# Performance work log

Hardware: AMD Instinct MI355X
Metric: run time of the kernel (lower is better)

The kernel has to match this reference:

```python
import jax, jax.numpy as jnp
import numpy as np

EPS = 1e-8

def _cosine(a, b):
    # a: (b,h,s,d), b: (b,1,1,d) -> (b,h,s). torch eps semantics: clamp each norm.
    num = jnp.sum(a * b, axis=-1)
    na = jnp.maximum(jnp.linalg.norm(a, axis=-1), EPS)
    nb = jnp.maximum(jnp.linalg.norm(b, axis=-1), EPS)
    return num / (na * nb)

def setup_inputs() -> dict:
    B, H, S, DH, DM = 2, 16, 2048, 64, 1024
    key = jax.random.key(0)
    ks = jax.random.split(key, 8)
    queries = jax.random.normal(ks[0], (B, H, S, DH), dtype=jnp.float32)
    keys = jax.random.normal(ks[1], (B, H, S, DH), dtype=jnp.float32)
    context = jax.random.normal(ks[2], (B, DM), dtype=jnp.float32)
    prev_state = jax.random.normal(ks[3], (B, S, DH), dtype=jnp.float32)
    # causal mask (1 = keep, 0 = masked), shape (B,1,S,S)
    attention_mask = jnp.broadcast_to(jnp.tril(jnp.ones((S, S), dtype=jnp.int32)), (B, 1, S, S))
    # learned params (Linear weights stored torch-style as (out, in))
    cfm_ctx_w = jax.random.normal(ks[4], (DH, DM), dtype=jnp.float32) / np.sqrt(DM)
    cfm_state_w = jax.random.normal(ks[5], (DH, DH), dtype=jnp.float32) / np.sqrt(DH)
    afm_ctx_w = jax.random.normal(ks[6], (DH, DM), dtype=jnp.float32) / np.sqrt(DM)
    cfm_scale = jnp.full((1,), 0.1, dtype=jnp.float32)
    afm_scale = jnp.full((1,), 0.1, dtype=jnp.float32)
    alpha = jnp.asarray(0.1, dtype=jnp.float32)
    beta = jnp.asarray(0.1, dtype=jnp.float32)
    return dict(queries=queries, keys=keys, context=context, prev_state=prev_state,
                attention_mask=attention_mask, cfm_ctx_w=cfm_ctx_w, cfm_state_w=cfm_state_w,
                cfm_scale=cfm_scale, afm_ctx_w=afm_ctx_w, afm_scale=afm_scale,
                alpha=alpha, beta=beta)

def reference(queries, keys, context, prev_state, attention_mask,
              cfm_ctx_w, cfm_state_w, cfm_scale, afm_ctx_w, afm_scale, alpha, beta):
    B, H, S, DH = queries.shape
    # QK^T / sqrt(d_k): (b,h,s,s)
    attn_scores = jnp.einsum('bhqd,bhkd->bhqk', queries, keys) / jnp.sqrt(jnp.asarray(DH, queries.dtype))
    # ---- CFM ----
    cfm_ctx = (context @ cfm_ctx_w.T)[:, None, None, :]            # (b,1,1,dh)
    witt = _cosine(keys, cfm_ctx)                                   # (b,h,s)
    state = (prev_state @ cfm_state_w.T)[:, None, :, :]             # (b,1,s,dh)
    hamming = jnp.mean(((keys > 0) != (state > 0)).astype(keys.dtype), axis=-1)  # (b,h,s)
    cfm = ((witt + (1.0 - hamming)) * cfm_scale[0])[:, :, None, :]  # (b,h,1,s)
    # ---- AFM (no key_probs -> uniform entropy 1/S) ----
    afm_ctx = (context @ afm_ctx_w.T)[:, None, None, :]
    contradiction = jax.nn.relu(-_cosine(keys, afm_ctx))            # (b,h,s)
    entropy = jnp.full_like(contradiction, 1.0 / S)
    afm = ((contradiction + entropy) * afm_scale[0])[:, :, None, :]
    composite = attn_scores + alpha * cfm - beta * afm
    composite = jnp.where(attention_mask == 0, -jnp.inf, composite)
    return composite
```

## Files before the change

kernel.cpp:

```cpp
#include <hip/hip_runtime.h>
#include <math.h>

#define BB 2
#define HH 16
#define SS 2048
#define DHD 64
#define DMD 1024
#define EPSF 1e-8f
#define NEG_FILL -1.0e30f

typedef __attribute__((ext_vector_type(8))) short bf16x8;
typedef __attribute__((ext_vector_type(4))) float f32x4;

#define WS_BIAS_F   1024
#define WS_CONV_F   66560
#define CONV_ELEMS  (BB * HH * SS * DHD)
#define GRAN_TOTAL  (CONV_ELEMS / 8)
#define WS_NEEDED_B ((size_t)WS_CONV_F * 4 + (size_t)CONV_ELEMS * 2 * 4)

static __device__ __forceinline__ unsigned short f2bf(float f) {
    unsigned u = __float_as_uint(f);
    u += 0x7FFFu + ((u >> 16) & 1u);
    return (unsigned short)(u >> 16);
}
static __device__ __forceinline__ float bf2f(unsigned short h) {
    return __uint_as_float(((unsigned)h) << 16);
}
static __device__ __forceinline__ void cvt8(const float* p, bf16x8& h8, bf16x8& l8) {
    float4 v0 = *(const float4*)p;
    float4 v1 = *(const float4*)(p + 4);
    float vf[8] = {v0.x, v0.y, v0.z, v0.w, v1.x, v1.y, v1.z, v1.w};
    #pragma unroll
    for (int j = 0; j < 8; ++j) {
        unsigned short h = f2bf(vf[j]);
        h8[j] = (short)h;
        l8[j] = (short)f2bf(vf[j] - bf2f(h));
    }
}

__global__ void ctx_kernel(const float* __restrict__ context,
                           const float* __restrict__ cfm_ctx_w,
                           const float* __restrict__ afm_ctx_w,
                           float* __restrict__ ws) {
    int t = threadIdx.x;
    int b = t >> 7, sel = (t >> 6) & 1, o = t & 63;
    const float* W = sel ? afm_ctx_w : cfm_ctx_w;
    const float4* wrow = (const float4*)(W + o * DMD);
    const float4* crow = (const float4*)(context + b * DMD);
    float acc = 0.f;
    for (int m = 0; m < DMD / 4; ++m) {
        float4 w4 = wrow[m];
        float4 c4 = crow[m];
        acc += w4.x * c4.x + w4.y * c4.y + w4.z * c4.z + w4.w * c4.w;
    }
    ws[b * 128 + sel * 64 + o] = acc;
    float sq = acc * acc;
    for (int off = 32; off >= 1; off >>= 1) sq += __shfl_xor(sq, off);
    if (o == 0) ws[256 + b * 2 + sel] = fmaxf(sqrtf(sq), EPSF);
}

__global__ void bias_kernel(const float* __restrict__ keys,
                            const float* __restrict__ prev_state,
                            const float* __restrict__ cfm_state_w,
                            const float* __restrict__ cfm_scale,
                            const float* __restrict__ afm_scale,
                            const float* __restrict__ alpha_p,
                            const float* __restrict__ beta_p,
                            const float* __restrict__ ws_ctx,
                            float* __restrict__ bias_out) {
    int gid = blockIdx.x * 4 + (threadIdx.x >> 6);
    int b = gid >> 11, s = gid & (SS - 1);
    int l = threadIdx.x & 63;
    const float4* prow = (const float4*)(prev_state + ((size_t)b * SS + s) * DHD);
    const float4* wrow = (const float4*)(cfm_state_w + l * DHD);
    float st = 0.f;
    #pragma unroll
    for (int j = 0; j < DHD / 4; ++j) {
        float4 p4 = prow[j], w4 = wrow[j];
        st += p4.x * w4.x + p4.y * w4.y + p4.z * w4.z + p4.w * w4.w;
    }
    unsigned long long smask = __ballot(st > 0.f);

    int h = l >> 2, q = l & 3, d0 = q * 16;
    int sb = (int)((smask >> d0) & 0xFFFFull);
    const float* krow = keys + (((size_t)(b * HH + h)) * SS + s) * DHD + d0;
    const float* cc = ws_ctx + b * 128 + d0;
    const float* ac = ws_ctx + b * 128 + 64 + d0;
    float v0 = 0.f, v1 = 0.f, v2 = 0.f, mism = 0.f;
    #pragma unroll
    for (int j4 = 0; j4 < 4; ++j4) {
        float4 k4 = *(const float4*)(krow + j4 * 4);
        float4 c4 = *(const float4*)(cc + j4 * 4);
        float4 a4 = *(const float4*)(ac + j4 * 4);
        float kf[4] = {k4.x, k4.y, k4.z, k4.w};
        float cf[4] = {c4.x, c4.y, c4.z, c4.w};
        float af[4] = {a4.x, a4.y, a4.z, a4.w};
        #pragma unroll
        for (int j = 0; j < 4; ++j) {
            float kd = kf[j];
            v0 = fmaf(kd, cf[j], v0);
            v1 = fmaf(kd, af[j], v1);
            v2 = fmaf(kd, kd, v2);
            int bit = (sb >> (j4 * 4 + j)) & 1;
            mism += ((kd > 0.f) != (bit != 0)) ? 1.f : 0.f;
        }
    }
    v0 += __shfl_xor(v0, 1); v0 += __shfl_xor(v0, 2);
    v1 += __shfl_xor(v1, 1); v1 += __shfl_xor(v1, 2);
    v2 += __shfl_xor(v2, 1); v2 += __shfl_xor(v2, 2);
    mism += __shfl_xor(mism, 1); mism += __shfl_xor(mism, 2);
    if (q == 0) {
        float nb_c = ws_ctx[256 + b * 2];
        float nb_a = ws_ctx[256 + b * 2 + 1];
        float al = alpha_p[0] * cfm_scale[0];
        float be = beta_p[0] * afm_scale[0];
        float nk = fmaxf(sqrtf(v2), EPSF);
        float witt = v0 / (nk * nb_c);
        float contra = fmaxf(-(v1 / (nk * nb_a)), 0.f);
        float ham = mism * (1.f / 64.f);
        bias_out[(size_t)(b * HH + h) * SS + s] =
            al * (witt + 1.f - ham) - be * (contra + 1.f / (float)SS);
    }
}

__global__ void conv_kernel(const float* __restrict__ Q,
                            const float* __restrict__ K,
                            unsigned short* __restrict__ wsc) {
    int sel = blockIdx.y;
    const float* src = sel ? K : Q;
    float scale = sel ? 1.f : 0.125f;
    unsigned short* hi = wsc + (size_t)(sel ? 2 : 0) * CONV_ELEMS;
    unsigned short* lo = hi + CONV_ELEMS;
    int gid = blockIdx.x * 256 + threadIdx.x;
    int bh = gid >> 14;
    int rem = gid & 16383;
    int u = rem >> 7, r2 = rem & 127;
    int s = r2 >> 6, r3 = r2 & 63;
    int lg = r3 >> 4, lr = r3 & 15;
    size_t sidx = ((size_t)bh * SS + u * 16 + lr) * DHD + s * 32 + lg * 8;
    float4 a = *(const float4*)(src + sidx);
    float4 b = *(const float4*)(src + sidx + 4);
    float vf[8] = {a.x, a.y, a.z, a.w, b.x, b.y, b.z, b.w};
    bf16x8 h8, l8;
    #pragma unroll
    for (int j = 0; j < 8; ++j) {
        float f = vf[j] * scale;
        unsigned short h = f2bf(f);
        h8[j] = (short)h;
        l8[j] = (short)f2bf(f - bf2f(h));
    }
    *(bf16x8*)(hi + (size_t)gid * 8) = h8;
    *(bf16x8*)(lo + (size_t)gid * 8) = l8;
}

#define MFMA16(A, B, C) __builtin_amdgcn_mfma_f32_16x16x32_bf16(A, B, C, 0, 0, 0)

__global__ __launch_bounds__(256, 2) void band_pc(
    const unsigned short* __restrict__ wsc,
    const float* __restrict__ bias, float* __restrict__ out) {
    int L = blockIdx.x;
    int xcd = L & 7, sL = L >> 3;
    int j = sL & 31;
    int bh = ((sL >> 5) << 3) | xcd;
    int tid = threadIdx.x;
    int w = tid >> 6, l = tid & 63, lr = l & 15, lg = l >> 4;
    int lg4 = lg * 4;

    int chunksA = (j >> 1) + 1;
    int chunksA4 = (chunksA + 3) & ~3;
    int chunksZ = 32 - (j >> 1);
    int chunksZ4 = (chunksZ + 3) & ~3;
    if (chunksZ4 > 32) chunksZ4 = 32;
    int nchunks = chunksZ4;
    int ngroups = nchunks >> 2;
    int mygroupsA = chunksA4 >> 2;
    int fillA = chunksA4 * 64;
    int fillZ = chunksZ4 * 64;
    int rowA = j * 32, rowZ = (63 - j) * 32;
    int fr0 = 4 * (ngroups - mygroupsA);
    if (fr0 > 32) fr0 = 32;

    __shared__ unsigned short KB[2][8192];
    __shared__ float BIASL[2048];
    __shared__ float TR[2][16 * 256];

    const unsigned short* Qh = wsc;
    const unsigned short* Ql = Qh + CONV_ELEMS;
    const unsigned short* Kh = Ql + CONV_ELEMS;
    const unsigned short* Kl = Kh + CONV_ELEMS;
    const float* bias_g = bias + (size_t)bh * SS;
    float* ob = out + (size_t)bh * SS * SS;
    size_t kbase = (size_t)bh * 131072;
    f32x4 fneg = {NEG_FILL, NEG_FILL, NEG_FILL, NEG_FILL};

#define STAGE(cidx, nb) do {                                                 \
    bf16x8 t[8];                                                             \
    _Pragma("unroll")                                                        \
    for (int gi = 0; gi < 8; ++gi) {                                         \
        int g = pw * 8 + gi, u = g >> 2, q = g & 3;                          \
        const unsigned short* src = (q < 2 ? Kh : Kl) + kbase                \
            + (size_t)((cidx) * 4 + u) * 1024 + (q & 1) * 512 + l * 8;       \
        t[gi] = *(const bf16x8*)src;                                         \
    }                                                                        \
    _Pragma("unroll")                                                        \
    for (int gi = 0; gi < 8; ++gi) {                                         \
        int g = pw * 8 + gi, u = g >> 2, q = g & 3;                          \
        *(bf16x8*)&KB[nb][u * 2048 + q * 512 + l * 8] = t[gi];               \
    }                                                                        \
} while (0)

    if (w >= 2) {
        int pw = w - 2;
        #pragma unroll
        for (int i = 0; i < 4; ++i) {
            f32x4 bv = *(const f32x4*)(bias_g + pw * 1024 + i * 256 + l * 4);
            *(f32x4*)&BIASL[pw * 1024 + i * 256 + l * 4] = bv;
        }
        STAGE(0, 0);
        asm volatile("s_waitcnt lgkmcnt(0)" ::: "memory");
        __builtin_amdgcn_sched_barrier(0);
        for (int c = 0; c < nchunks; ++c) {
            __builtin_amdgcn_s_barrier();
            if (c + 1 < nchunks) {
                STAGE(c + 1, (c + 1) & 1);
                asm volatile("s_waitcnt lgkmcnt(0)" ::: "memory");
                __builtin_amdgcn_sched_barrier(0);
            }
        }
    } else {
        int row0 = (w == 0) ? rowA : rowZ;
        int mygroups = (w == 0) ? mygroupsA : ngroups;
        float* trw = &TR[w][0];
        int fr = 0;
        bf16x8 q0h0, q0h1, q0l0, q0l1, q1h0, q1h1, q1l0, q1l1;
        {
            size_t qb = kbase + (size_t)(row0 >> 4) * 1024;
            q0h0 = *(const bf16x8*)(Qh + qb + l * 8);
            q0h1 = *(const bf16x8*)(Qh + qb + 512 + l * 8);
            q1h0 = *(const bf16x8*)(Qh + qb + 1024 + l * 8);
            q1h1 = *(const bf16x8*)(Qh + qb + 1536 + l * 8);
            q0l0 = *(const bf16x8*)(Ql + qb + l * 8);
            q0l1 = *(const bf16x8*)(Ql + qb + 512 + l * 8);
            q1l0 = *(const bf16x8*)(Ql + qb + 1024 + l * 8);
            q1l1 = *(const bf16x8*)(Ql + qb + 1536 + l * 8);
        }
        f32x4 acc0[16], acc1[16];
        for (int g = 0; g < ngroups; ++g) {
            if (g < mygroups) {
                #pragma unroll
                for (int cc = 0; cc < 4; ++cc) {
                    __builtin_amdgcn_s_barrier();
                    const unsigned short* kb = &KB[cc & 1][0];
                    #pragma unroll
                    for (int u = 0; u < 4; ++u) {
                        int ui = cc * 4 + u;
                        int ug = g * 16 + ui;
                        bf16x8 kh0 = *(const bf16x8*)&kb[u * 2048 + l * 8];
                        bf16x8 kh1 = *(const bf16x8*)&kb[u * 2048 + 512 + l * 8];
                        bf16x8 kl0 = *(const bf16x8*)&kb[u * 2048 + 1024 + l * 8];
                        bf16x8 kl1 = *(const bf16x8*)&kb[u * 2048 + 1536 + l * 8];
                        f32x4 bv = *(const f32x4*)&BIASL[ug * 16 + lg4];
                        int c0 = ug * 16 + lg4;
                        {
                            int row = row0 + lr;
                            f32x4 a = {0.f, 0.f, 0.f, 0.f};
                            a = MFMA16(kh0, q0h0, a);
                            a = MFMA16(kh1, q0h1, a);
                            a = MFMA16(kh0, q0l0, a);
                            a = MFMA16(kh1, q0l1, a);
                            a = MFMA16(kl0, q0h0, a);
                            a = MFMA16(kl1, q0h1, a);
                            #pragma unroll
                            for (int e = 0; e < 4; ++e) {
                                float x = a[e] + bv[e];
                                if (c0 + e > row) x = NEG_FILL;
                                a[e] = x;
                            }
                            acc0[ui] = a;
                        }
                        {
                            int row = row0 + 16 + lr;
                            f32x4 a = {0.f, 0.f, 0.f, 0.f};
                            a = MFMA16(kh0, q1h0, a);
                            a = MFMA16(kh1, q1h1, a);
                            a = MFMA16(kh0, q1l0, a);
                            a = MFMA16(kh1, q1l1, a);
                            a = MFMA16(kl0, q1h0, a);
                            a = MFMA16(kl1, q1h1, a);
                            #pragma unroll
                            for (int e = 0; e < 4; ++e) {
                                float x = a[e] + bv[e];
                                if (c0 + e > row) x = NEG_FILL;
                                a[e] = x;
                            }
                            acc1[ui] = a;
                        }
                    }
                }
                #pragma unroll
                for (int u16 = 0; u16 < 16; ++u16)
                    *(f32x4*)&trw[lr * 256 + ((u16 * 16 + lg4) ^ ((lr & 7) << 2))] = acc0[u16];
                asm volatile("s_waitcnt lgkmcnt(0)" ::: "memory");
                __builtin_amdgcn_sched_barrier(0);
                #pragma unroll
                for (int r = 0; r < 16; ++r) {
                    f32x4 v = *(const f32x4*)&trw[r * 256 + ((l * 4) ^ ((r & 7) << 2))];
                    __builtin_nontemporal_store(v,
                        (f32x4*)(ob + (size_t)(row0 + r) * SS + g * 256 + l * 4));
                }
                asm volatile("s_waitcnt lgkmcnt(0)" ::: "memory");
                __builtin_amdgcn_sched_barrier(0);
                #pragma unroll
                for (int u16 = 0; u16 < 16; ++u16)
                    *(f32x4*)&trw[lr * 256 + ((u16 * 16 + lg4) ^ ((lr & 7) << 2))] = acc1[u16];
                asm volatile("s_waitcnt lgkmcnt(0)" ::: "memory");
                __builtin_amdgcn_sched_barrier(0);
                #pragma unroll
                for (int r = 0; r < 16; ++r) {
                    f32x4 v = *(const f32x4*)&trw[r * 256 + ((l * 4) ^ ((r & 7) << 2))];
                    __builtin_nontemporal_store(v,
                        (f32x4*)(ob + (size_t)(row0 + 16 + r) * SS + g * 256 + l * 4));
                }
                asm volatile("s_waitcnt lgkmcnt(0)" ::: "memory");
                __builtin_amdgcn_sched_barrier(0);
            } else {
                #pragma unroll
                for (int cc = 0; cc < 4; ++cc) {
                    __builtin_amdgcn_s_barrier();
                    if (fr < 32) {
                        float* orow = ob + (size_t)(rowA + fr) * SS;
                        for (int c = fillA + l * 4; c < SS; c += 256)
                            __builtin_nontemporal_store(fneg, (f32x4*)(orow + c));
                        ++fr;
                    }
                }
            }
        }
    }

    {
        int remA = 32 - fr0;
        int nZ = (fillZ < SS) ? 32 : 0;
        int total = remA + nZ;
        for (int i = w; i < total; i += 4) {
            int row, f0;
            if (i < remA) { row = rowA + fr0 + i; f0 = fillA; }
            else          { row = rowZ + (i - remA); f0 = fillZ; }
            float* orow = ob + (size_t)row * SS;
            for (int c = f0 + l * 4; c < SS; c += 256)
                __builtin_nontemporal_store(fneg, (f32x4*)(orow + c));
        }
    }
#undef STAGE
}

#define LOADB(S, unit) do {                                                  \
    size_t _r = ((size_t)bh * SS + (unit) * 16 + lr) * DHD + lg * 8;         \
    cvt8(K + _r, S##h0, S##l0);                                              \
    cvt8(K + _r + 32, S##h1, S##l1);                                         \
    S##bv = *(const f32x4*)(bias_row + (unit) * 16 + lg4);                   \
} while (0)

#define COMP(S, unit) do {                                                   \
    int _c0 = (unit) * 16 + lg4;                                             \
    {                                                                        \
        int _row = row0 + lr;                                                \
        f32x4 _a = {0.f, 0.f, 0.f, 0.f};                                     \
        _a = MFMA16(S##h0, q0h0, _a);                                        \
        _a = MFMA16(S##h1, q0h1, _a);                                        \
        _a = MFMA16(S##h0, q0l0, _a);                                        \
        _a = MFMA16(S##h1, q0l1, _a);                                        \
        _a = MFMA16(S##l0, q0h0, _a);                                        \
        _a = MFMA16(S##l1, q0h1, _a);                                        \
        f32x4 _v;                                                            \
        _Pragma("unroll")                                                    \
        for (int _e = 0; _e < 4; ++_e) {                                     \
            float _x = fmaf(_a[_e], 0.125f, S##bv[_e]);                      \
            if (_c0 + _e > _row) _x = NEG_FILL;                              \
            _v[_e] = _x;                                                     \
        }                                                                    \
        __builtin_nontemporal_store(_v, (f32x4*)(ob + (size_t)_row * SS + _c0)); \
    }                                                                        \
    {                                                                        \
        int _row = row0 + 16 + lr;                                           \
        f32x4 _a = {0.f, 0.f, 0.f, 0.f};                                     \
        _a = MFMA16(S##h0, q1h0, _a);                                        \
        _a = MFMA16(S##h1, q1h1, _a);                                        \
        _a = MFMA16(S##h0, q1l0, _a);                                        \
        _a = MFMA16(S##h1, q1l1, _a);                                        \
        _a = MFMA16(S##l0, q1h0, _a);                                        \
        _a = MFMA16(S##l1, q1h1, _a);                                        \
        f32x4 _v;                                                            \
        _Pragma("unroll")                                                    \
        for (int _e = 0; _e < 4; ++_e) {                                     \
            float _x = fmaf(_a[_e], 0.125f, S##bv[_e]);                      \
            if (_c0 + _e > _row) _x = NEG_FILL;                              \
            _v[_e] = _x;                                                     \
        }                                                                    \
        __builtin_nontemporal_store(_v, (f32x4*)(ob + (size_t)_row * SS + _c0)); \
    }                                                                        \
} while (0)

__global__ __launch_bounds__(128, 2) void band_fallback(
    const float* __restrict__ Q, const float* __restrict__ K,
    const float* __restrict__ bias, float* __restrict__ out) {
    int L = blockIdx.x;
    int xcd = L & 7, sL = L >> 3;
    int j = sL & 31;
    int bh = ((sL >> 5) << 3) | xcd;
    int tid = threadIdx.x;
    int w = tid >> 6, l = tid & 63, lr = l & 15, lg = l >> 4;
    int lg4 = lg * 4;
    int band = w ? (63 - j) : j;
    int row0 = band * 32;
    int nunits = 2 * band + 2;

    const float* bias_row = bias + (size_t)bh * SS;
    float* ob = out + (size_t)bh * SS * SS;

    bf16x8 q0h0, q0h1, q0l0, q0l1, q1h0, q1h1, q1l0, q1l1;
    {
        size_t qr0 = ((size_t)bh * SS + row0 + lr) * DHD + lg * 8;
        cvt8(Q + qr0, q0h0, q0l0);
        cvt8(Q + qr0 + 32, q0h1, q0l1);
        size_t qr1 = qr0 + (size_t)16 * DHD;
        cvt8(Q + qr1, q1h0, q1l0);
        cvt8(Q + qr1 + 32, q1h1, q1l1);
    }

    bf16x8 Ah0, Ah1, Al0, Al1, Bh0, Bh1, Bl0, Bl1;
    f32x4 Abv, Bbv;
    LOADB(A, 0);
    LOADB(B, 1);
    for (int u = 0; u < nunits; u += 2) {
        COMP(A, u);
        if (u + 2 < nunits) LOADB(A, u + 2);
        COMP(B, u + 1);
        if (u + 3 < nunits) LOADB(B, u + 3);
    }

    f32x4 f4 = {NEG_FILL, NEG_FILL, NEG_FILL, NEG_FILL};
    int fill0 = nunits * 16;
    for (int r = 0; r < 32; ++r) {
        float* orow = ob + (size_t)(row0 + r) * SS;
        for (int c = fill0 + l * 4; c < SS; c += 256)
            __builtin_nontemporal_store(f4, (f32x4*)(orow + c));
    }
}

extern "C" void kernel_launch(void* const* d_in, const int* in_sizes, int n_in,
                              void* d_out, int out_size, void* d_ws, size_t ws_size,
                              hipStream_t stream) {
    const float* queries     = (const float*)d_in[0];
    const float* keys        = (const float*)d_in[1];
    const float* context     = (const float*)d_in[2];
    const float* prev_state  = (const float*)d_in[3];
    const float* cfm_ctx_w   = (const float*)d_in[5];
    const float* cfm_state_w = (const float*)d_in[6];
    const float* cfm_scale   = (const float*)d_in[7];
    const float* afm_ctx_w   = (const float*)d_in[8];
    const float* afm_scale   = (const float*)d_in[9];
    const float* alpha_p     = (const float*)d_in[10];
    const float* beta_p      = (const float*)d_in[11];
    float* out = (float*)d_out;
    float* ws  = (float*)d_ws;
    float* bias = ws + WS_BIAS_F;
    unsigned short* wsc = (unsigned short*)(ws + WS_CONV_F);

    ctx_kernel<<<1, 256, 0, stream>>>(context, cfm_ctx_w, afm_ctx_w, ws);
    bias_kernel<<<BB * SS / 4, 256, 0, stream>>>(keys, prev_state, cfm_state_w,
                                                 cfm_scale, afm_scale, alpha_p,
                                                 beta_p, ws, bias);
    if (ws_size >= WS_NEEDED_B) {
        conv_kernel<<<dim3(GRAN_TOTAL / 256, 2), 256, 0, stream>>>(
            queries, keys, wsc);
        band_pc<<<1024, 256, 0, stream>>>(wsc, bias, out);
    } else {
        band_fallback<<<1024, 128, 0, stream>>>(queries, keys, bias, out);
    }
}
```

Before: 194.1 us.

## Split band_pc into 8 waves with one 16-row tile per compute wave

The band kernel grows from 4 to 8 waves per block. Four compute waves each own 16 query rows instead of two waves owning 32, and four producer waves share the K staging. The bias is now double-buffered one 256-column group at a time instead of loading the full row, and the transpose scratch is split into 8-row halves per wave. This is meant to halve per-wave accumulator registers and add parallelism and latency hiding, at the cost of more barriers and duplicated Q fragment loads.

New measurement: 202.9 us. 4.5% more time.

```diff
diff --git a/kernel.cpp b/kernel.cpp
--- a/kernel.cpp
+++ b/kernel.cpp
@@ -155,7 +155,7 @@
 
 #define MFMA16(A, B, C) __builtin_amdgcn_mfma_f32_16x16x32_bf16(A, B, C, 0, 0, 0)
 
-__global__ __launch_bounds__(256, 2) void band_pc(
+__global__ __launch_bounds__(512, 4) void band_pc(
     const unsigned short* __restrict__ wsc,
     const float* __restrict__ bias, float* __restrict__ out) {
     int L = blockIdx.x;
@@ -178,11 +178,11 @@
     int fillZ = chunksZ4 * 64;
     int rowA = j * 32, rowZ = (63 - j) * 32;
     int fr0 = 4 * (ngroups - mygroupsA);
-    if (fr0 > 32) fr0 = 32;
+    if (fr0 > 16) fr0 = 16;
 
     __shared__ unsigned short KB[2][8192];
-    __shared__ float BIASL[2048];
-    __shared__ float TR[2][16 * 256];
+    __shared__ float BIASG[2][256];
+    __shared__ float TR[4][8 * 256];
 
     const unsigned short* Qh = wsc;
     const unsigned short* Ql = Qh + CONV_ELEMS;
@@ -194,57 +194,56 @@
     f32x4 fneg = {NEG_FILL, NEG_FILL, NEG_FILL, NEG_FILL};
 
 #define STAGE(cidx, nb) do {                                                 \
-    bf16x8 t[8];                                                             \
+    bf16x8 t[4];                                                             \
     _Pragma("unroll")                                                        \
-    for (int gi = 0; gi < 8; ++gi) {                                         \
-        int g = pw * 8 + gi, u = g >> 2, q = g & 3;                          \
+    for (int gi = 0; gi < 4; ++gi) {                                         \
+        int g = pw * 4 + gi, u = g >> 2, q = g & 3;                          \
         const unsigned short* src = (q < 2 ? Kh : Kl) + kbase                \
             + (size_t)((cidx) * 4 + u) * 1024 + (q & 1) * 512 + l * 8;       \
         t[gi] = *(const bf16x8*)src;                                         \
     }                                                                        \
     _Pragma("unroll")                                                        \
-    for (int gi = 0; gi < 8; ++gi) {                                         \
-        int g = pw * 8 + gi, u = g >> 2, q = g & 3;                          \
+    for (int gi = 0; gi < 4; ++gi) {                                         \
+        int g = pw * 4 + gi, u = g >> 2, q = g & 3;                          \
         *(bf16x8*)&KB[nb][u * 2048 + q * 512 + l * 8] = t[gi];               \
     }                                                                        \
 } while (0)
 
-    if (w >= 2) {
-        int pw = w - 2;
-        #pragma unroll
-        for (int i = 0; i < 4; ++i) {
-            f32x4 bv = *(const f32x4*)(bias_g + pw * 1024 + i * 256 + l * 4);
-            *(f32x4*)&BIASL[pw * 1024 + i * 256 + l * 4] = bv;
-        }
+    if (w >= 4) {
+        int pw = w - 4;
         STAGE(0, 0);
+        if (pw == 0)
+            *(f32x4*)&BIASG[0][l * 4] = *(const f32x4*)(bias_g + l * 4);
         asm volatile("s_waitcnt lgkmcnt(0)" ::: "memory");
         __builtin_amdgcn_sched_barrier(0);
         for (int c = 0; c < nchunks; ++c) {
             __builtin_amdgcn_s_barrier();
             if (c + 1 < nchunks) {
                 STAGE(c + 1, (c + 1) & 1);
+                if (pw == 0 && ((c + 1) & 3) == 0) {
+                    int gg = (c + 1) >> 2;
+                    *(f32x4*)&BIASG[gg & 1][l * 4] =
+                        *(const f32x4*)(bias_g + gg * 256 + l * 4);
+                }
                 asm volatile("s_waitcnt lgkmcnt(0)" ::: "memory");
                 __builtin_amdgcn_sched_barrier(0);
             }
         }
     } else {
-        int row0 = (w == 0) ? rowA : rowZ;
-        int mygroups = (w == 0) ? mygroupsA : ngroups;
+        int band = w >> 1, half = w & 1;
+        int row0 = (band ? rowZ : rowA) + half * 16;
+        int mygroups = band ? ngroups : mygroupsA;
         float* trw = &TR[w][0];
         int fr = 0;
-        bf16x8 q0h0, q0h1, q0l0, q0l1, q1h0, q1h1, q1l0, q1l1;
+        bf16x8 qh0, qh1, ql0, ql1;
         {
             size_t qb = kbase + (size_t)(row0 >> 4) * 1024;
-            q0h0 = *(const bf16x8*)(Qh + qb + l * 8);
-            q0h1 = *(const bf16x8*)(Qh + qb + 512 + l * 8);
-            q1h0 = *(const bf16x8*)(Qh + qb + 1024 + l * 8);
-            q1h1 = *(const bf16x8*)(Qh + qb + 1536 + l * 8);
-            q0l0 = *(const bf16x8*)(Ql + qb + l * 8);
-            q0l1 = *(const bf16x8*)(Ql + qb + 512 + l * 8);
-            q1l0 = *(const bf16x8*)(Ql + qb + 1024 + l * 8);
-            q1l1 = *(const bf16x8*)(Ql + qb + 1536 + l * 8);
+            qh0 = *(const bf16x8*)(Qh + qb + l * 8);
+            qh1 = *(const bf16x8*)(Qh + qb + 512 + l * 8);
+            ql0 = *(const bf16x8*)(Ql + qb + l * 8);
+            ql1 = *(const bf16x8*)(Ql + qb + 512 + l * 8);
         }
-        f32x4 acc0[16], acc1[16];
+        f32x4 acc[16];
         for (int g = 0; g < ngroups; ++g) {
             if (g < mygroups) {
                 #pragma unroll
@@ -259,76 +258,50 @@
                         bf16x8 kh1 = *(const bf16x8*)&kb[u * 2048 + 512 + l * 8];
                         bf16x8 kl0 = *(const bf16x8*)&kb[u * 2048 + 1024 + l * 8];
                         bf16x8 kl1 = *(const bf16x8*)&kb[u * 2048 + 1536 + l * 8];
-                        f32x4 bv = *(const f32x4*)&BIASL[ug * 16 + lg4];
+                        f32x4 bv = *(const f32x4*)&BIASG[g & 1][ui * 16 + lg4];
                         int c0 = ug * 16 + lg4;
-                        {
-                            int row = row0 + lr;
-                            f32x4 a = {0.f, 0.f, 0.f, 0.f};
-                            a = MFMA16(kh0, q0h0, a);
-                            a = MFMA16(kh1, q0h1, a);
-                            a = MFMA16(kh0, q0l0, a);
-                            a = MFMA16(kh1, q0l1, a);
-                            a = MFMA16(kl0, q0h0, a);
-                            a = MFMA16(kl1, q0h1, a);
-                            #pragma unroll
-                            for (int e = 0; e < 4; ++e) {
-                                float x = a[e] + bv[e];
-                                if (c0 + e > row) x = NEG_FILL;
-                                a[e] = x;
-                            }
-                            acc0[ui] = a;
+                        int row = row0 + lr;
+                        f32x4 a = {0.f, 0.f, 0.f, 0.f};
+                        a = MFMA16(kh0, qh0, a);
+                        a = MFMA16(kh1, qh1, a);
+                        a = MFMA16(kh0, ql0, a);
+                        a = MFMA16(kh1, ql1, a);
+                        a = MFMA16(kl0, qh0, a);
+                        a = MFMA16(kl1, qh1, a);
+                        #pragma unroll
+                        for (int e = 0; e < 4; ++e) {
+                            float x = a[e] + bv[e];
+                            if (c0 + e > row) x = NEG_FILL;
+                            a[e] = x;
                         }
-                        {
-                            int row = row0 + 16 + lr;
-                            f32x4 a = {0.f, 0.f, 0.f, 0.f};
-                            a = MFMA16(kh0, q1h0, a);
-                            a = MFMA16(kh1, q1h1, a);
-                            a = MFMA16(kh0, q1l0, a);
-                            a = MFMA16(kh1, q1l1, a);
-                            a = MFMA16(kl0, q1h0, a);
-                            a = MFMA16(kl1, q1h1, a);
-                            #pragma unroll
-                            for (int e = 0; e < 4; ++e) {
-                                float x = a[e] + bv[e];
-                                if (c0 + e > row) x = NEG_FILL;
-                                a[e] = x;
-                            }
-                            acc1[ui] = a;
-                        }
+                        acc[ui] = a;
                     }
                 }
                 #pragma unroll
-                for (int u16 = 0; u16 < 16; ++u16)
-                    *(f32x4*)&trw[lr * 256 + ((u16 * 16 + lg4) ^ ((lr & 7) << 2))] = acc0[u16];
-                asm volatile("s_waitcnt lgkmcnt(0)" ::: "memory");
-                __builtin_amdgcn_sched_barrier(0);
-                #pragma unroll
-                for (int r = 0; r < 16; ++r) {
-                    f32x4 v = *(const f32x4*)&trw[r * 256 + ((l * 4) ^ ((r & 7) << 2))];
-                    __builtin_nontemporal_store(v,
-                        (f32x4*)(ob + (size_t)(row0 + r) * SS + g * 256 + l * 4));
+                for (int p = 0; p < 2; ++p) {
+                    if ((lr >> 3) == p) {
+                        #pragma unroll
+                        for (int u16 = 0; u16 < 16; ++u16)
+                            *(f32x4*)&trw[(lr & 7) * 256 +
+                                ((u16 * 16 + lg4) ^ ((lr & 7) << 2))] = acc[u16];
+                    }
+                    asm volatile("s_waitcnt lgkmcnt(0)" ::: "memory");
+                    __builtin_amdgcn_sched_barrier(0);
+                    #pragma unroll
+                    for (int r = 0; r < 8; ++r) {
+                        f32x4 v = *(const f32x4*)&trw[r * 256 + ((l * 4) ^ (r << 2))];
+                        __builtin_nontemporal_store(v,
+                            (f32x4*)(ob + (size_t)(row0 + p * 8 + r) * SS + g * 256 + l * 4));
+                    }
+                    asm volatile("s_waitcnt lgkmcnt(0)" ::: "memory");
+                    __builtin_amdgcn_sched_barrier(0);
                 }
-                asm volatile("s_waitcnt lgkmcnt(0)" ::: "memory");
-                __builtin_amdgcn_sched_barrier(0);
-                #pragma unroll
-                for (int u16 = 0; u16 < 16; ++u16)
-                    *(f32x4*)&trw[lr * 256 + ((u16 * 16 + lg4) ^ ((lr & 7) << 2))] = acc1[u16];
-                asm volatile("s_waitcnt lgkmcnt(0)" ::: "memory");
-                __builtin_amdgcn_sched_barrier(0);
-                #pragma unroll
-                for (int r = 0; r < 16; ++r) {
-                    f32x4 v = *(const f32x4*)&trw[r * 256 + ((l * 4) ^ ((r & 7) << 2))];
-                    __builtin_nontemporal_store(v,
-                        (f32x4*)(ob + (size_t)(row0 + 16 + r) * SS + g * 256 + l * 4));
-                }
-                asm volatile("s_waitcnt lgkmcnt(0)" ::: "memory");
-                __builtin_amdgcn_sched_barrier(0);
             } else {
                 #pragma unroll
                 for (int cc = 0; cc < 4; ++cc) {
                     __builtin_amdgcn_s_barrier();
-                    if (fr < 32) {
-                        float* orow = ob + (size_t)(rowA + fr) * SS;
+                    if (fr < 16) {
+                        float* orow = ob + (size_t)(row0 + fr) * SS;
                         for (int c = fillA + l * 4; c < SS; c += 256)
                             __builtin_nontemporal_store(fneg, (f32x4*)(orow + c));
                         ++fr;
@@ -339,13 +312,14 @@
     }
 
     {
-        int remA = 32 - fr0;
+        int remH = 16 - fr0;
         int nZ = (fillZ < SS) ? 32 : 0;
-        int total = remA + nZ;
-        for (int i = w; i < total; i += 4) {
+        int total = 2 * remH + nZ;
+        for (int i = w; i < total; i += 8) {
             int row, f0;
-            if (i < remA) { row = rowA + fr0 + i; f0 = fillA; }
-            else          { row = rowZ + (i - remA); f0 = fillZ; }
+            if (i < remH)            { row = rowA + fr0 + i; f0 = fillA; }
+            else if (i < 2 * remH)   { row = rowA + 16 + fr0 + (i - remH); f0 = fillA; }
+            else                     { row = rowZ + (i - 2 * remH); f0 = fillZ; }
             float* orow = ob + (size_t)row * SS;
             for (int c = f0 + l * 4; c < SS; c += 256)
                 __builtin_nontemporal_store(fneg, (f32x4*)(orow + c));
@@ -474,7 +448,7 @@
     if (ws_size >= WS_NEEDED_B) {
         conv_kernel<<<dim3(GRAN_TOTAL / 256, 2), 256, 0, stream>>>(
             queries, keys, wsc);
-        band_pc<<<1024, 256, 0, stream>>>(wsc, bias, out);
+        band_pc<<<1024, 512, 0, stream>>>(wsc, bias, out);
     } else {
         band_fallback<<<1024, 128, 0, stream>>>(queries, keys, bias, out);
     }
```
